# Kernel optimization log

Measured on AMD Instinct MI355X. Metric: run time of the kernel, lower is better.

The kernel has to match this reference:

```python
import jax, jax.numpy as jnp
import numpy as np

H = 512

def _lstm_dir(seq, Wih, Whh, bih, bhh, reverse):
    # seq: [B,S,in]; Wih: [4H,in]; Whh: [4H,H]; biases [4H]
    B = seq.shape[0]
    xp = jnp.einsum('bsi,gi->bsg', seq, Wih) + bih  # precompute input projection [B,S,4H]
    h0 = jnp.zeros((B, H), seq.dtype)
    c0 = jnp.zeros((B, H), seq.dtype)

    def step(carry, xt):
        h, c = carry
        g = xt + h @ Whh.T + bhh
        i, f, gg, o = jnp.split(g, 4, axis=-1)
        c = jax.nn.sigmoid(f) * c + jax.nn.sigmoid(i) * jnp.tanh(gg)
        h = jax.nn.sigmoid(o) * jnp.tanh(c)
        return (h, c), h

    _, hs = jax.lax.scan(step, (h0, c0), jnp.swapaxes(xp, 0, 1), reverse=reverse)
    return jnp.swapaxes(hs, 0, 1)  # [B,S,H]


def setup_inputs() -> dict:
    key = jax.random.key(0)
    ks = jax.random.split(key, 24)
    B, S, E, V, C = 32, 512, 512, 32000, 2
    sc = 0.1
    d = {
        'x': jax.random.randint(ks[0], (B, S), 0, V, dtype=jnp.int32),
        'attention_mask': jnp.ones((B, S), dtype=jnp.int32),
        'emb': jax.random.normal(ks[1], (V, E), jnp.float32) * sc,
        'fc_W': jax.random.normal(ks[2], (C, 2 * H), jnp.float32) * sc,
        'fc_b': jax.random.normal(ks[3], (C,), jnp.float32) * sc,
    }
    i = 4
    for l, insz in [(0, E), (1, 2 * H)]:
        for dname in ('fwd', 'bwd'):
            d[f'{dname}_Wih{l}'] = jax.random.normal(ks[i], (4 * H, insz), jnp.float32) * sc; i += 1
            d[f'{dname}_Whh{l}'] = jax.random.normal(ks[i], (4 * H, H), jnp.float32) * sc; i += 1
            d[f'{dname}_bih{l}'] = jax.random.normal(ks[i], (4 * H,), jnp.float32) * sc; i += 1
            d[f'{dname}_bhh{l}'] = jax.random.normal(ks[i], (4 * H,), jnp.float32) * sc; i += 1
    return d


def reference(x, attention_mask, emb, fc_W, fc_b,
              fwd_Wih0, fwd_Whh0, fwd_bih0, fwd_bhh0,
              bwd_Wih0, bwd_Whh0, bwd_bih0, bwd_bhh0,
              fwd_Wih1, fwd_Whh1, fwd_bih1, fwd_bhh1,
              bwd_Wih1, bwd_Whh1, bwd_bih1, bwd_bhh1):
    out = emb[x]  # [B,S,E]
    layers = [
        ((fwd_Wih0, fwd_Whh0, fwd_bih0, fwd_bhh0), (bwd_Wih0, bwd_Whh0, bwd_bih0, bwd_bhh0)),
        ((fwd_Wih1, fwd_Whh1, fwd_bih1, fwd_bhh1), (bwd_Wih1, bwd_Whh1, bwd_bih1, bwd_bhh1)),
    ]
    for fw, bw in layers:
        f = _lstm_dir(out, *fw, reverse=False)
        b = _lstm_dir(out, *bw, reverse=True)
        out = jnp.concatenate([f, b], axis=-1)  # [B,S,2H]
        # dropout is identity in eval mode
    mask = attention_mask.astype(out.dtype)
    pooled = (out * mask[..., None]).sum(axis=1) / jnp.clip(mask.sum(axis=1, keepdims=True), 1e-9)
    logits = pooled @ fc_W.T + fc_b
    return logits
```

## Files before the change

kernel.cpp:

```cpp
#include <hip/hip_runtime.h>

typedef unsigned short u16;
typedef unsigned int   u32;
typedef unsigned long long u64;
typedef __attribute__((ext_vector_type(8))) short bf16x8;
typedef __attribute__((ext_vector_type(4))) float f32x4;

__device__ __forceinline__ u16 f2bf(float f) {
    u32 u; __builtin_memcpy(&u, &f, 4);
    u32 r = (u + 0x7FFFu + ((u >> 16) & 1u)) >> 16;
    return (u16)r;
}
__device__ __forceinline__ float bf2f(u16 h) {
    u32 u = ((u32)h) << 16; float f; __builtin_memcpy(&f, &u, 4); return f;
}
__device__ __forceinline__ float sigmoidf(float x) { return 1.f / (1.f + __expf(-x)); }
__device__ __forceinline__ float tanh_safe(float x) {
    float e = __expf(-2.f * fabsf(x));
    float t = (1.f - e) / (1.f + e);
    return x >= 0.f ? t : -t;
}

__global__ __launch_bounds__(256) void castk2(const float* __restrict__ s, u16* __restrict__ hi,
                                              u16* __restrict__ lo, int n) {
    int i = blockIdx.x * 256 + threadIdx.x;
    if (i < n) {
        float f = s[i];
        u16 h = f2bf(f);
        hi[i] = h;
        lo[i] = f2bf(f - bf2f(h));
    }
}

__global__ __launch_bounds__(256) void embed_cast(const int* __restrict__ x, const float* __restrict__ emb,
                                                  u16* __restrict__ x0) {
    int m = blockIdx.x;
    int idx = x[m];
    const float2* src = (const float2*)(emb + (size_t)idx * 512);
    u16* dst = x0 + (size_t)m * 512;
    int t = threadIdx.x;
    float2 v = src[t];
    dst[t * 2]     = f2bf(v.x);
    dst[t * 2 + 1] = f2bf(v.y);
}

__global__ __launch_bounds__(256) void gemm_bt(const u16* __restrict__ A, const u16* __restrict__ Bhi,
                                               const u16* __restrict__ Blo,
                                               u16* __restrict__ C, int M, int N, int K) {
    __shared__ __align__(16) u16 sA[128 * 32];
    __shared__ __align__(16) u16 sBh[128 * 32];
    __shared__ __align__(16) u16 sBl[128 * 32];
    const int tid  = threadIdx.x;
    const int lane = tid & 63, wave = tid >> 6;
    const int m0 = blockIdx.y * 128, n0 = blockIdx.x * 128;
    const int wm = (wave >> 1) * 64, wn = (wave & 1) * 64;
    f32x4 acc[4][4] = {};

    const int r0 = tid >> 2, c8 = (tid & 3) * 8;
    const int r1 = r0 + 64;
    const u16* Ap   = A   + (size_t)(m0 + r0) * K + c8;
    const u16* Ap2  = A   + (size_t)(m0 + r1) * K + c8;
    const u16* Bhp  = Bhi + (size_t)(n0 + r0) * K + c8;
    const u16* Bhp2 = Bhi + (size_t)(n0 + r1) * K + c8;
    const u16* Blp  = Blo + (size_t)(n0 + r0) * K + c8;
    const u16* Blp2 = Blo + (size_t)(n0 + r1) * K + c8;

    uint4 ra0, ra1, rh0, rh1, rl0, rl1;
    ra0 = *(const uint4*)(Ap);   ra1 = *(const uint4*)(Ap2);
    rh0 = *(const uint4*)(Bhp);  rh1 = *(const uint4*)(Bhp2);
    rl0 = *(const uint4*)(Blp);  rl1 = *(const uint4*)(Blp2);

    for (int kk = 0; kk < K; kk += 32) {
        __syncthreads();
        *(uint4*)(sA  + tid * 8)        = ra0;
        *(uint4*)(sA  + 2048 + tid * 8) = ra1;
        *(uint4*)(sBh + tid * 8)        = rh0;
        *(uint4*)(sBh + 2048 + tid * 8) = rh1;
        *(uint4*)(sBl + tid * 8)        = rl0;
        *(uint4*)(sBl + 2048 + tid * 8) = rl1;
        int kn = kk + 32;
        if (kn < K) {
            ra0 = *(const uint4*)(Ap + kn);   ra1 = *(const uint4*)(Ap2 + kn);
            rh0 = *(const uint4*)(Bhp + kn);  rh1 = *(const uint4*)(Bhp2 + kn);
            rl0 = *(const uint4*)(Blp + kn);  rl1 = *(const uint4*)(Blp2 + kn);
        }
        __syncthreads();
        bf16x8 av[4], bh[4], bl[4];
#pragma unroll
        for (int i = 0; i < 4; ++i) {
            av[i] = *(const bf16x8*)(sA  + (wm + i * 16 + (lane & 15)) * 32 + (lane >> 4) * 8);
            bh[i] = *(const bf16x8*)(sBh + (wn + i * 16 + (lane & 15)) * 32 + (lane >> 4) * 8);
            bl[i] = *(const bf16x8*)(sBl + (wn + i * 16 + (lane & 15)) * 32 + (lane >> 4) * 8);
        }
#pragma unroll
        for (int i = 0; i < 4; ++i)
#pragma unroll
            for (int j = 0; j < 4; ++j) {
                acc[i][j] = __builtin_amdgcn_mfma_f32_16x16x32_bf16(av[i], bh[j], acc[i][j], 0, 0, 0);
                acc[i][j] = __builtin_amdgcn_mfma_f32_16x16x32_bf16(av[i], bl[j], acc[i][j], 0, 0, 0);
            }
    }
#pragma unroll
    for (int i = 0; i < 4; ++i) {
        int m = m0 + wm + i * 16 + ((lane >> 4) << 2);
#pragma unroll
        for (int j = 0; j < 4; ++j) {
            int n = n0 + wn + j * 16 + (lane & 15);
#pragma unroll
            for (int rr = 0; rr < 4; ++rr)
                C[(size_t)(m + rr) * N + n] = f2bf(acc[i][j][rr]);
        }
    }
}

template <int LAYER>
__global__ __launch_bounds__(256, 1) void lstm_rec(
    const u16* __restrict__ xp_f, const u16* __restrict__ xp_b,
    const u16* __restrict__ whh_f_hi, const u16* __restrict__ whh_f_lo,
    const u16* __restrict__ whh_b_hi, const u16* __restrict__ whh_b_lo,
    const float* __restrict__ bih_f, const float* __restrict__ bhh_f,
    const float* __restrict__ bih_b, const float* __restrict__ bhh_b,
    u16* __restrict__ out0, float* __restrict__ pooled, const int* __restrict__ mask,
    u16* hbuf, u32* cnt)
{
    const int HP = 520;
    __shared__ __align__(16) u16  sHhi[32 * 520];
    __shared__ __align__(16) u16  sHlo[32 * 520];
    __shared__ __align__(16) u16  sXp[32 * 32];
    __shared__ __align__(16) float sG[32 * 33];
    __shared__ __align__(16) u16  sHoutHi[32 * 8];
    __shared__ __align__(16) u16  sHoutLo[32 * 8];

    const int tid = threadIdx.x;
    const int dir = blockIdx.x >> 6;
    const int slice = blockIdx.x & 63;
    const u16* xp     = dir ? xp_b : xp_f;
    const u16* whhH   = dir ? whh_b_hi : whh_f_hi;
    const u16* whhL   = dir ? whh_b_lo : whh_f_lo;
    const float* bih  = dir ? bih_b : bih_f;
    const float* bhh  = dir ? bhh_b : bhh_f;
    u16* hbD = hbuf + dir * 65536;
    u32* myCnt = cnt + dir * 64;

    const int wave = tid >> 6, lane = tid & 63;
    const int wm = (wave >> 1) * 16;
    const int wn = (wave & 1) * 16;
    bf16x8 wfragH[16], wfragL[16];
    {
        int n = wn + (lane & 15);
        int q = n >> 3, rr = n & 7;
        size_t rowoff = (size_t)(q * 512 + slice * 8 + rr) * 512 + (lane >> 4) * 8;
        const u16* wrh = whhH + rowoff;
        const u16* wrl = whhL + rowoff;
#pragma unroll
        for (int k2 = 0; k2 < 16; ++k2) {
            wfragH[k2] = *(const bf16x8*)(wrh + k2 * 32);
            wfragL[k2] = *(const bf16x8*)(wrl + k2 * 32);
        }
    }
    const int b = tid >> 3, r = tid & 7;
    float bias[4];
#pragma unroll
    for (int q = 0; q < 4; ++q) {
        int g = q * 512 + slice * 8 + r;
        bias[q] = bih[g] + bhh[g];
    }
    float cstate = 0.f, pool = 0.f;
    const int aoff = (wm + (lane & 15)) * HP + (lane >> 4) * 8;
    const int gRow = wm + ((lane >> 4) << 2), gCol = wn + (lane & 15);
    const int srow = tid >> 3, sc = tid & 7;

    for (int t = 0; t < 512; ++t) {
        const int tt = dir ? (511 - t) : t;
        if (tid < 128) {
            int xb = tid >> 2, xq = tid & 3;
            const uint4 v = *(const uint4*)(xp + ((size_t)(xb * 512 + tt)) * 2048 + xq * 512 + slice * 8);
            *(uint4*)(sXp + xb * 32 + xq * 8) = v;
        }
        if (t > 0) {
            if (tid == 0) {
                u32 tgt = 64u * (u32)t;
                while (__hip_atomic_load(myCnt, __ATOMIC_RELAXED, __HIP_MEMORY_SCOPE_AGENT) < tgt)
                    __builtin_amdgcn_s_sleep(1);
            }
            __syncthreads();
            {
                const u16* hp = hbD + ((t - 1) & 1) * 32768 + srow * 512;
                const u16* lp = hp + 16384;
                u16* dhi = sHhi + srow * HP;
                u16* dlo = sHlo + srow * HP;
#pragma unroll
                for (int j = 0; j < 8; ++j) {
                    int ch = sc + 8 * j;
                    u64 a0 = __hip_atomic_load((const u64*)(hp + ch * 8),     __ATOMIC_RELAXED, __HIP_MEMORY_SCOPE_AGENT);
                    u64 a1 = __hip_atomic_load((const u64*)(hp + ch * 8) + 1, __ATOMIC_RELAXED, __HIP_MEMORY_SCOPE_AGENT);
                    u64 b0 = __hip_atomic_load((const u64*)(lp + ch * 8),     __ATOMIC_RELAXED, __HIP_MEMORY_SCOPE_AGENT);
                    u64 b1 = __hip_atomic_load((const u64*)(lp + ch * 8) + 1, __ATOMIC_RELAXED, __HIP_MEMORY_SCOPE_AGENT);
                    *(u64*)(dhi + ch * 8)     = a0;
                    *(u64*)(dhi + ch * 8 + 4) = a1;
                    *(u64*)(dlo + ch * 8)     = b0;
                    *(u64*)(dlo + ch * 8 + 4) = b1;
                }
            }
        }
        __syncthreads();
        f32x4 acc = {};
        if (t > 0) {
#pragma unroll
            for (int k2 = 0; k2 < 16; ++k2) {
                bf16x8 ah = *(const bf16x8*)(sHhi + aoff + k2 * 32);
                bf16x8 al = *(const bf16x8*)(sHlo + aoff + k2 * 32);
                acc = __builtin_amdgcn_mfma_f32_16x16x32_bf16(ah, wfragH[k2], acc, 0, 0, 0);
                acc = __builtin_amdgcn_mfma_f32_16x16x32_bf16(al, wfragH[k2], acc, 0, 0, 0);
                acc = __builtin_amdgcn_mfma_f32_16x16x32_bf16(ah, wfragL[k2], acc, 0, 0, 0);
            }
        }
#pragma unroll
        for (int rr = 0; rr < 4; ++rr) sG[(gRow + rr) * 33 + gCol] = acc[rr];
        __syncthreads();
        {
            float gq[4];
#pragma unroll
            for (int q = 0; q < 4; ++q)
                gq[q] = sG[b * 33 + q * 8 + r] + bf2f(sXp[b * 32 + q * 8 + r]) + bias[q];
            float ig = sigmoidf(gq[0]), fg = sigmoidf(gq[1]);
            float gg = tanh_safe(gq[2]), og = sigmoidf(gq[3]);
            cstate = fg * cstate + ig * gg;
            float h = og * tanh_safe(cstate);
            u16 hh = f2bf(h);
            if (LAYER == 0) {
                out0[((size_t)(b * 512 + tt)) * 1024 + dir * 512 + slice * 8 + r] = hh;
            } else {
                pool += h * (float)mask[b * 512 + tt];
            }
            sHoutHi[b * 8 + r] = hh;
            sHoutLo[b * 8 + r] = f2bf(h - bf2f(hh));
        }
        __syncthreads();
        if (tid < 128) {
            int w = tid;
            int pb = w >> 2, d = w & 3;
            u32 vh = ((const u32*)sHoutHi)[w];
            u32 vl = ((const u32*)sHoutLo)[w];
            u32* gh = (u32*)(hbD + (t & 1) * 32768 + pb * 512 + slice * 8) + d;
            u32* gl = (u32*)(hbD + (t & 1) * 32768 + 16384 + pb * 512 + slice * 8) + d;
            __hip_atomic_store(gh, vh, __ATOMIC_RELAXED, __HIP_MEMORY_SCOPE_AGENT);
            __hip_atomic_store(gl, vl, __ATOMIC_RELAXED, __HIP_MEMORY_SCOPE_AGENT);
        }
        __syncthreads();
        if (tid == 0)
            __hip_atomic_fetch_add(myCnt, 1u, __ATOMIC_RELEASE, __HIP_MEMORY_SCOPE_AGENT);
    }
    if (LAYER == 1)
        pooled[(size_t)b * 1024 + dir * 512 + slice * 8 + r] = pool;
}

__global__ __launch_bounds__(256) void final_fc(const float* __restrict__ pooled, const int* __restrict__ mask,
                                                const float* __restrict__ fcW, const float* __restrict__ fcb,
                                                float* __restrict__ out) {
    __shared__ float red[256];
    int tid = threadIdx.x;
    int pair = tid & 63, kc = tid >> 6;
    int b = pair >> 1, c = pair & 1;
    float s = 0.f;
    for (int k = kc * 256; k < kc * 256 + 256; ++k)
        s += pooled[b * 1024 + k] * fcW[c * 1024 + k];
    red[tid] = s;
    __syncthreads();
    if (kc == 0) {
        float tot = red[pair] + red[64 + pair] + red[128 + pair] + red[192 + pair];
        float ms = 0.f;
        for (int t = 0; t < 512; ++t) ms += (float)mask[b * 512 + t];
        ms = fmaxf(ms, 1e-9f);
        out[b * 2 + c] = tot / ms + fcb[c];
    }
}

extern "C" void kernel_launch(void* const* d_in, const int* in_sizes, int n_in,
                              void* d_out, int out_size, void* d_ws, size_t ws_size,
                              hipStream_t stream) {
    (void)in_sizes; (void)n_in; (void)out_size; (void)ws_size;
    const int*   x     = (const int*)d_in[0];
    const int*   amask = (const int*)d_in[1];
    const float* emb   = (const float*)d_in[2];
    const float* fcW   = (const float*)d_in[3];
    const float* fcb   = (const float*)d_in[4];
    const float* fWih0 = (const float*)d_in[5];
    const float* fWhh0 = (const float*)d_in[6];
    const float* fbih0 = (const float*)d_in[7];
    const float* fbhh0 = (const float*)d_in[8];
    const float* bWih0 = (const float*)d_in[9];
    const float* bWhh0 = (const float*)d_in[10];
    const float* bbih0 = (const float*)d_in[11];
    const float* bbhh0 = (const float*)d_in[12];
    const float* fWih1 = (const float*)d_in[13];
    const float* fWhh1 = (const float*)d_in[14];
    const float* fbih1 = (const float*)d_in[15];
    const float* fbhh1 = (const float*)d_in[16];
    const float* bWih1 = (const float*)d_in[17];
    const float* bWhh1 = (const float*)d_in[18];
    const float* bbih1 = (const float*)d_in[19];
    const float* bbhh1 = (const float*)d_in[20];

    char* ws = (char*)d_ws;
    size_t off = 0;
    auto alloc = [&](size_t bytes) { void* p = ws + off; off += (bytes + 1023) & ~(size_t)1023; return p; };
    u16* x0    = (u16*)alloc((size_t)16384 * 512 * 2);
    u16* xpf   = (u16*)alloc((size_t)16384 * 2048 * 2);
    u16* xpb   = (u16*)alloc((size_t)16384 * 2048 * 2);
    u16* out0  = (u16*)alloc((size_t)16384 * 1024 * 2);
    u16* wih0fH = (u16*)alloc((size_t)2048 * 512 * 2);
    u16* wih0fL = (u16*)alloc((size_t)2048 * 512 * 2);
    u16* wih0bH = (u16*)alloc((size_t)2048 * 512 * 2);
    u16* wih0bL = (u16*)alloc((size_t)2048 * 512 * 2);
    u16* whh0fH = (u16*)alloc((size_t)2048 * 512 * 2);
    u16* whh0fL = (u16*)alloc((size_t)2048 * 512 * 2);
    u16* whh0bH = (u16*)alloc((size_t)2048 * 512 * 2);
    u16* whh0bL = (u16*)alloc((size_t)2048 * 512 * 2);
    u16* wih1fH = (u16*)alloc((size_t)2048 * 1024 * 2);
    u16* wih1fL = (u16*)alloc((size_t)2048 * 1024 * 2);
    u16* wih1bH = (u16*)alloc((size_t)2048 * 1024 * 2);
    u16* wih1bL = (u16*)alloc((size_t)2048 * 1024 * 2);
    u16* whh1fH = (u16*)alloc((size_t)2048 * 512 * 2);
    u16* whh1fL = (u16*)alloc((size_t)2048 * 512 * 2);
    u16* whh1bH = (u16*)alloc((size_t)2048 * 512 * 2);
    u16* whh1bL = (u16*)alloc((size_t)2048 * 512 * 2);
    float* pooled = (float*)alloc((size_t)32 * 1024 * 4);
    u16* hbuf  = (u16*)alloc((size_t)2 * 2 * 2 * 32 * 512 * 2);
    u32* cnt   = (u32*)alloc(1024);

    hipMemsetAsync(cnt, 0, 1024, stream);

    const int NW0 = 2048 * 512, NW1 = 2048 * 1024;
    castk2<<<dim3((NW0 + 255) / 256), 256, 0, stream>>>(fWih0, wih0fH, wih0fL, NW0);
    castk2<<<dim3((NW0 + 255) / 256), 256, 0, stream>>>(bWih0, wih0bH, wih0bL, NW0);
    castk2<<<dim3((NW0 + 255) / 256), 256, 0, stream>>>(fWhh0, whh0fH, whh0fL, NW0);
    castk2<<<dim3((NW0 + 255) / 256), 256, 0, stream>>>(bWhh0, whh0bH, whh0bL, NW0);
    castk2<<<dim3((NW1 + 255) / 256), 256, 0, stream>>>(fWih1, wih1fH, wih1fL, NW1);
    castk2<<<dim3((NW1 + 255) / 256), 256, 0, stream>>>(bWih1, wih1bH, wih1bL, NW1);
    castk2<<<dim3((NW0 + 255) / 256), 256, 0, stream>>>(fWhh1, whh1fH, whh1fL, NW0);
    castk2<<<dim3((NW0 + 255) / 256), 256, 0, stream>>>(bWhh1, whh1bH, whh1bL, NW0);

    embed_cast<<<dim3(16384), 256, 0, stream>>>(x, emb, x0);

    gemm_bt<<<dim3(16, 128), 256, 0, stream>>>(x0, wih0fH, wih0fL, xpf, 16384, 2048, 512);
    gemm_bt<<<dim3(16, 128), 256, 0, stream>>>(x0, wih0bH, wih0bL, xpb, 16384, 2048, 512);
    lstm_rec<0><<<dim3(128), 256, 0, stream>>>(xpf, xpb, whh0fH, whh0fL, whh0bH, whh0bL,
                                               fbih0, fbhh0, bbih0, bbhh0,
                                               out0, nullptr, nullptr, hbuf, cnt);
    gemm_bt<<<dim3(16, 128), 256, 0, stream>>>(out0, wih1fH, wih1fL, xpf, 16384, 2048, 1024);
    gemm_bt<<<dim3(16, 128), 256, 0, stream>>>(out0, wih1bH, wih1bL, xpb, 16384, 2048, 1024);
    lstm_rec<1><<<dim3(128), 256, 0, stream>>>(xpf, xpb, whh1fH, whh1fL, whh1bH, whh1bL,
                                               fbih1, fbhh1, bbih1, bbhh1,
                                               nullptr, pooled, amask, hbuf, cnt + 128);

    final_fc<<<dim3(1), 256, 0, stream>>>(pooled, amask, fcW, fcb, (float*)d_out);
}
```

Baseline: 7.702 ms.

## Replace shared atomic step counter with per-slice flags and wave-wide polling

Each of the 64 slices now writes its own progress flag with a release store, instead of all slices doing fetch_add on one counter. Consumers poll all 64 flags in parallel from one wave and use __all to decide when to proceed. The handoff loads of h are issued together before their LDS stores to overlap latency. The h publish is done by a single wave, which drops one block-wide barrier per step. The aim is less atomic contention and lower per-step cross-block barrier latency, at the cost of more polling loads and reliance on the release ordering covering the other lanes of the wave.

```diff
diff --git a/kernel.cpp b/kernel.cpp
--- a/kernel.cpp
+++ b/kernel.cpp
@@ -140,7 +140,7 @@
     const float* bih  = dir ? bih_b : bih_f;
     const float* bhh  = dir ? bhh_b : bhh_f;
     u16* hbD = hbuf + dir * 65536;
-    u32* myCnt = cnt + dir * 64;
+    u32* myFlags = cnt + dir * 64;
 
     const int wave = tid >> 6, lane = tid & 63;
     const int wm = (wave >> 1) * 16;
@@ -177,30 +177,36 @@
             const uint4 v = *(const uint4*)(xp + ((size_t)(xb * 512 + tt)) * 2048 + xq * 512 + slice * 8);
             *(uint4*)(sXp + xb * 32 + xq * 8) = v;
         }
+        if (t > 0 && tid < 64) {
+            const u32 tgt = (u32)t;
+            for (;;) {
+                u32 v = __hip_atomic_load(myFlags + tid, __ATOMIC_RELAXED, __HIP_MEMORY_SCOPE_AGENT);
+                if (__all((int)(v >= tgt))) break;
+                __builtin_amdgcn_s_sleep(1);
+            }
+        }
+        __syncthreads();
         if (t > 0) {
-            if (tid == 0) {
-                u32 tgt = 64u * (u32)t;
-                while (__hip_atomic_load(myCnt, __ATOMIC_RELAXED, __HIP_MEMORY_SCOPE_AGENT) < tgt)
-                    __builtin_amdgcn_s_sleep(1);
-            }
-            __syncthreads();
-            {
-                const u16* hp = hbD + ((t - 1) & 1) * 32768 + srow * 512;
-                const u16* lp = hp + 16384;
-                u16* dhi = sHhi + srow * HP;
-                u16* dlo = sHlo + srow * HP;
-#pragma unroll
-                for (int j = 0; j < 8; ++j) {
-                    int ch = sc + 8 * j;
-                    u64 a0 = __hip_atomic_load((const u64*)(hp + ch * 8),     __ATOMIC_RELAXED, __HIP_MEMORY_SCOPE_AGENT);
-                    u64 a1 = __hip_atomic_load((const u64*)(hp + ch * 8) + 1, __ATOMIC_RELAXED, __HIP_MEMORY_SCOPE_AGENT);
-                    u64 b0 = __hip_atomic_load((const u64*)(lp + ch * 8),     __ATOMIC_RELAXED, __HIP_MEMORY_SCOPE_AGENT);
-                    u64 b1 = __hip_atomic_load((const u64*)(lp + ch * 8) + 1, __ATOMIC_RELAXED, __HIP_MEMORY_SCOPE_AGENT);
-                    *(u64*)(dhi + ch * 8)     = a0;
-                    *(u64*)(dhi + ch * 8 + 4) = a1;
-                    *(u64*)(dlo + ch * 8)     = b0;
-                    *(u64*)(dlo + ch * 8 + 4) = b1;
-                }
+            const u16* hp = hbD + ((t - 1) & 1) * 32768 + srow * 512;
+            const u16* lp = hp + 16384;
+            u16* dhi = sHhi + srow * HP;
+            u16* dlo = sHlo + srow * HP;
+            u64 rh[16], rl[16];
+#pragma unroll
+            for (int j = 0; j < 8; ++j) {
+                int ch = sc + 8 * j;
+                rh[2*j]   = __hip_atomic_load((const u64*)(hp + ch * 8),     __ATOMIC_RELAXED, __HIP_MEMORY_SCOPE_AGENT);
+                rh[2*j+1] = __hip_atomic_load((const u64*)(hp + ch * 8) + 1, __ATOMIC_RELAXED, __HIP_MEMORY_SCOPE_AGENT);
+                rl[2*j]   = __hip_atomic_load((const u64*)(lp + ch * 8),     __ATOMIC_RELAXED, __HIP_MEMORY_SCOPE_AGENT);
+                rl[2*j+1] = __hip_atomic_load((const u64*)(lp + ch * 8) + 1, __ATOMIC_RELAXED, __HIP_MEMORY_SCOPE_AGENT);
+            }
+#pragma unroll
+            for (int j = 0; j < 8; ++j) {
+                int ch = sc + 8 * j;
+                *(u64*)(dhi + ch * 8)     = rh[2*j];
+                *(u64*)(dhi + ch * 8 + 4) = rh[2*j+1];
+                *(u64*)(dlo + ch * 8)     = rl[2*j];
+                *(u64*)(dlo + ch * 8 + 4) = rl[2*j+1];
             }
         }
         __syncthreads();
@@ -237,19 +243,21 @@
             sHoutLo[b * 8 + r] = f2bf(h - bf2f(hh));
         }
         __syncthreads();
-        if (tid < 128) {
-            int w = tid;
-            int pb = w >> 2, d = w & 3;
-            u32 vh = ((const u32*)sHoutHi)[w];
-            u32 vl = ((const u32*)sHoutLo)[w];
-            u32* gh = (u32*)(hbD + (t & 1) * 32768 + pb * 512 + slice * 8) + d;
-            u32* gl = (u32*)(hbD + (t & 1) * 32768 + 16384 + pb * 512 + slice * 8) + d;
-            __hip_atomic_store(gh, vh, __ATOMIC_RELAXED, __HIP_MEMORY_SCOPE_AGENT);
-            __hip_atomic_store(gl, vl, __ATOMIC_RELAXED, __HIP_MEMORY_SCOPE_AGENT);
-        }
-        __syncthreads();
-        if (tid == 0)
-            __hip_atomic_fetch_add(myCnt, 1u, __ATOMIC_RELEASE, __HIP_MEMORY_SCOPE_AGENT);
+        if (tid < 64) {
+#pragma unroll
+            for (int j = 0; j < 2; ++j) {
+                int w = tid + 64 * j;
+                int pb = w >> 2, d = w & 3;
+                u32 vh = ((const u32*)sHoutHi)[w];
+                u32 vl = ((const u32*)sHoutLo)[w];
+                u32* gh = (u32*)(hbD + (t & 1) * 32768 + pb * 512 + slice * 8) + d;
+                u32* gl = (u32*)(hbD + (t & 1) * 32768 + 16384 + pb * 512 + slice * 8) + d;
+                __hip_atomic_store(gh, vh, __ATOMIC_RELAXED, __HIP_MEMORY_SCOPE_AGENT);
+                __hip_atomic_store(gl, vl, __ATOMIC_RELAXED, __HIP_MEMORY_SCOPE_AGENT);
+            }
+            if (tid == 0)
+                __hip_atomic_store(myFlags + slice, (u32)(t + 1), __ATOMIC_RELEASE, __HIP_MEMORY_SCOPE_AGENT);
+        }
     }
     if (LAYER == 1)
         pooled[(size_t)b * 1024 + dir * 512 + slice * 8 + r] = pool;
```

Measured after the change: 7.155 ms. 1.08x faster.
